# Kernel optimization log

Hardware: AMD Instinct MI355X
Metric: run time of the kernel (lower is better)

Reference implementation:

```python
import jax, jax.numpy as jnp
import numpy as np

D_MODEL = 1024
HEADS = 16
D_K = D_MODEL // HEADS


def setup_inputs() -> dict:
    key = jax.random.key(0)
    ks = jax.random.split(key, 11)
    B, S = 4, 2048
    s = 1.0 / np.sqrt(D_MODEL)
    return {
        "q": jax.random.normal(ks[0], (B, S, D_MODEL), dtype=jnp.float32),
        "k": jax.random.normal(ks[1], (B, S, D_MODEL), dtype=jnp.float32),
        "v": jax.random.normal(ks[2], (B, S, D_MODEL), dtype=jnp.float32),
        "Wq": jax.random.normal(ks[3], (D_MODEL, D_MODEL), dtype=jnp.float32) * s,
        "bq": jnp.zeros((D_MODEL,), dtype=jnp.float32),
        "Wk": jax.random.normal(ks[4], (D_MODEL, D_MODEL), dtype=jnp.float32) * s,
        "bk": jnp.zeros((D_MODEL,), dtype=jnp.float32),
        "Wv": jax.random.normal(ks[5], (D_MODEL, D_MODEL), dtype=jnp.float32) * s,
        "bv": jnp.zeros((D_MODEL,), dtype=jnp.float32),
        "Wo": jax.random.normal(ks[6], (D_MODEL, D_MODEL), dtype=jnp.float32) * s,
        "bo": jnp.zeros((D_MODEL,), dtype=jnp.float32),
    }


def reference(q, k, v, Wq, bq, Wk, bk, Wv, bv, Wo, bo):
    B, S, _ = q.shape
    # projections -> [B, H, S, d_k]
    def proj(x, W, b):
        return (x @ W.T + b).reshape(B, -1, HEADS, D_K).transpose(0, 2, 1, 3)
    qh = proj(q, Wq, bq)
    kh = proj(k, Wk, bk)
    vh = proj(v, Wv, bv)
    scores = jnp.einsum("bhqd,bhkd->bhqk", qh, kh) / jnp.sqrt(jnp.float32(D_K))
    attn = jax.nn.softmax(scores, axis=-1)  # dropout is identity in eval mode
    out = jnp.einsum("bhqk,bhkd->bhqd", attn, vh)
    concat = out.transpose(0, 2, 1, 3).reshape(B, S, D_MODEL)
    return concat @ Wo.T + bo
```

## Files before the change

kernel.cpp:

```cpp
#include <hip/hip_runtime.h>
#include <hip/hip_bf16.h>


typedef __attribute__((ext_vector_type(8))) short bf16x8;
typedef __attribute__((ext_vector_type(4))) float f32x4;
typedef __attribute__((ext_vector_type(4))) float fvec4;
typedef __attribute__((ext_vector_type(4))) unsigned int uvec4;
typedef __attribute__((ext_vector_type(4))) unsigned short usvec4;

#define MFMA16(a, b, c) __builtin_amdgcn_mfma_f32_16x16x32_bf16((a), (b), (c), 0, 0, 0)

static __device__ __forceinline__ unsigned short f2bf(float f) {
  unsigned u = __builtin_bit_cast(unsigned, f);
  unsigned r = u + 0x7FFFu + ((u >> 16) & 1u);
  return (unsigned short)(r >> 16);
}
static __device__ __forceinline__ float bf2f(unsigned short h) {
  unsigned u = ((unsigned)h) << 16;
  return __builtin_bit_cast(float, u);
}
static __device__ __forceinline__ void split2(float x, unsigned short& hi, unsigned short& lo) {
  hi = f2bf(x);
  lo = f2bf(x - bf2f(hi));
}
static __device__ __forceinline__ unsigned int split_pack(float x) {
  unsigned short hi, lo;
  split2(x, hi, lo);
  return ((unsigned)lo << 16) | (unsigned)hi;
}

static __device__ __forceinline__ int swz(int row, int col_us) {
  return (row << 6) + ((((col_us >> 3) ^ row) & 7) << 3) + (col_us & 7);
}

static __device__ __forceinline__ void glds16(const void* g, void* l) {
  __builtin_amdgcn_global_load_lds(
      (const __attribute__((address_space(1))) void*)g,
      (__attribute__((address_space(3))) void*)l, 16, 0, 0);
}

__global__ __launch_bounds__(256) void convert_split(
    const float* __restrict__ in, unsigned short* __restrict__ hp,
    unsigned short* __restrict__ lp, int n) {
  const int i = (blockIdx.x * 256 + threadIdx.x) * 4;
  if (i >= n) return;
  fvec4 x = *reinterpret_cast<const fvec4*>(&in[i]);
  usvec4 h, l;
#pragma unroll
  for (int j = 0; j < 4; ++j) {
    unsigned short hi, lo;
    split2(x[j], hi, lo);
    h[j] = hi; l[j] = lo;
  }
  *reinterpret_cast<usvec4*>(&hp[i]) = h;
  *reinterpret_cast<usvec4*>(&lp[i]) = l;
}

template <int AMODE, int BMODE, int OMODE>
__global__ __launch_bounds__(256) void gemm_k(
    const void* __restrict__ Ap0, const void* __restrict__ Ap1,
    const void* __restrict__ Bp0, const void* __restrict__ Bp1,
    const float* __restrict__ bias, void* __restrict__ Cout,
    int M, int N, int K) {
  __shared__ unsigned short Ahi[128 * 64], Alo[128 * 64];
  __shared__ unsigned short Bhi[128 * 64], Blo[128 * 64];

  const int t = threadIdx.x;
  const int l = t & 63;
  const int w = t >> 6;
  const int g = l >> 4;
  const int r16 = l & 15;
  const int wr = w >> 1, wc = w & 1;

  const int m0 = blockIdx.y * 128;
  const int n0 = blockIdx.x * 128;

  const int srow = t >> 4;
  const int scol = (t & 15) * 4;
  const int glrow = l >> 3;
  const int glcol = ((l & 7) ^ glrow) * 8;

  f32x4 acc[4][4];
#pragma unroll
  for (int m = 0; m < 4; ++m)
#pragma unroll
    for (int n = 0; n < 4; ++n) acc[m][n] = (f32x4){0.f, 0.f, 0.f, 0.f};

  const int ksteps = K / 64;
  for (int kt = 0; kt < ksteps; ++kt) {
    if constexpr (AMODE == 2) {
#pragma unroll
      for (int c = 0; c < 4; ++c) {
        const int row = (c * 4 + w) * 8 + glrow;
        const size_t go = (size_t)(m0 + row) * K + kt * 64 + glcol;
        glds16(&((const unsigned short*)Ap0)[go], &Ahi[(c * 4 + w) * 512]);
        glds16(&((const unsigned short*)Ap1)[go], &Alo[(c * 4 + w) * 512]);
      }
    }
    if constexpr (BMODE == 1) {
#pragma unroll
      for (int c = 0; c < 4; ++c) {
        const int row = (c * 4 + w) * 8 + glrow;
        const size_t go = (size_t)(n0 + row) * K + kt * 64 + glcol;
        glds16(&((const unsigned short*)Bp0)[go], &Bhi[(c * 4 + w) * 512]);
        glds16(&((const unsigned short*)Bp1)[go], &Blo[(c * 4 + w) * 512]);
      }
    }
    if constexpr (AMODE <= 1 || BMODE == 0) {
#pragma unroll
      for (int p = 0; p < 8; ++p) {
        const int row = srow + p * 16;
        const int o = swz(row, scol);
        if constexpr (AMODE == 0) {
          fvec4 av = *reinterpret_cast<const fvec4*>(
              &((const float*)Ap0)[(size_t)(m0 + row) * K + kt * 64 + scol]);
          usvec4 ah, al;
#pragma unroll
          for (int j = 0; j < 4; ++j) {
            unsigned short h, lo;
            split2(av[j], h, lo);
            ah[j] = h; al[j] = lo;
          }
          *reinterpret_cast<usvec4*>(&Ahi[o]) = ah;
          *reinterpret_cast<usvec4*>(&Alo[o]) = al;
        } else if constexpr (AMODE == 1) {
          uvec4 av = *reinterpret_cast<const uvec4*>(
              &((const unsigned int*)Ap0)[(size_t)(m0 + row) * K + kt * 64 + scol]);
          usvec4 ah, al;
#pragma unroll
          for (int j = 0; j < 4; ++j) {
            ah[j] = (unsigned short)(av[j] & 0xFFFFu);
            al[j] = (unsigned short)(av[j] >> 16);
          }
          *reinterpret_cast<usvec4*>(&Ahi[o]) = ah;
          *reinterpret_cast<usvec4*>(&Alo[o]) = al;
        }
        if constexpr (BMODE == 0) {
          fvec4 wv = *reinterpret_cast<const fvec4*>(
              &((const float*)Bp0)[(size_t)(n0 + row) * K + kt * 64 + scol]);
          usvec4 bh, bl;
#pragma unroll
          for (int j = 0; j < 4; ++j) {
            unsigned short h, lo;
            split2(wv[j], h, lo);
            bh[j] = h; bl[j] = lo;
          }
          *reinterpret_cast<usvec4*>(&Bhi[o]) = bh;
          *reinterpret_cast<usvec4*>(&Blo[o]) = bl;
        }
      }
    }
    __syncthreads();

#pragma unroll
    for (int ks = 0; ks < 2; ++ks) {
      bf16x8 ah[4], al[4], bh[4], bl[4];
#pragma unroll
      for (int m = 0; m < 4; ++m) {
        const int o = swz(wr * 64 + m * 16 + r16, ks * 32 + g * 8);
        ah[m] = *reinterpret_cast<const bf16x8*>(&Ahi[o]);
        al[m] = *reinterpret_cast<const bf16x8*>(&Alo[o]);
      }
#pragma unroll
      for (int n = 0; n < 4; ++n) {
        const int o = swz(wc * 64 + n * 16 + r16, ks * 32 + g * 8);
        bh[n] = *reinterpret_cast<const bf16x8*>(&Bhi[o]);
        bl[n] = *reinterpret_cast<const bf16x8*>(&Blo[o]);
      }
#pragma unroll
      for (int m = 0; m < 4; ++m)
#pragma unroll
        for (int n = 0; n < 4; ++n) {
          acc[m][n] = MFMA16(al[m], bh[n], acc[m][n]);
          acc[m][n] = MFMA16(ah[m], bl[n], acc[m][n]);
          acc[m][n] = MFMA16(ah[m], bh[n], acc[m][n]);
        }
    }
    __syncthreads();
  }

  float bv[4];
#pragma unroll
  for (int n = 0; n < 4; ++n) bv[n] = bias[n0 + wc * 64 + n * 16 + r16];

#pragma unroll
  for (int m = 0; m < 4; ++m)
#pragma unroll
    for (int n = 0; n < 4; ++n)
#pragma unroll
      for (int r = 0; r < 4; ++r) {
        const int row = m0 + wr * 64 + m * 16 + g * 4 + r;
        const int col = n0 + wc * 64 + n * 16 + r16;
        const float c = acc[m][n][r] + bv[n];
        if constexpr (OMODE == 0) {
          ((float*)Cout)[(size_t)row * N + col] = c;
        } else if constexpr (OMODE == 1) {
          ((unsigned int*)Cout)[(size_t)row * N + col] = split_pack(c);
        } else {
          ((unsigned int*)Cout)[(size_t)row * N + col] = split_pack(c * 0.125f);
        }
      }
}

template <int OPL>
__global__ __launch_bounds__(256) void attn_fwd(
    const unsigned int* Qpk, const unsigned int* __restrict__ Kpk,
    const unsigned int* __restrict__ Vpk, unsigned int* CtxPk,
    unsigned short* CtxH, unsigned short* CtxL, int S) {
  constexpr int DM = 1024, DK = 64;
  __shared__ unsigned short Khi[64 * 64], Klo[64 * 64];
  __shared__ unsigned short Vth[64 * 64], Vtl[64 * 64];
  __shared__ unsigned short Ph[4 * 16 * 64], Pl[4 * 16 * 64];

  const int t = threadIdx.x;
  const int l = t & 63;
  const int w = t >> 6;
  const int g = l >> 4;
  const int r16 = l & 15;
  const int pw = w << 10;

  const int b = blockIdx.z, h = blockIdx.y;
  const int q0 = blockIdx.x * 128;

  bf16x8 qhi[2][2], qlo[2][2];
#pragma unroll
  for (int qq = 0; qq < 2; ++qq)
#pragma unroll
    for (int ks = 0; ks < 2; ++ks) {
      const unsigned int* qrow =
          &Qpk[(size_t)(b * S + q0 + qq * 64 + w * 16 + r16) * DM + h * DK + ks * 32 + g * 8];
      uvec4 u0 = *reinterpret_cast<const uvec4*>(qrow);
      uvec4 u1 = *reinterpret_cast<const uvec4*>(qrow + 4);
#pragma unroll
      for (int j = 0; j < 4; ++j) {
        qhi[qq][ks][j] = (short)(u0[j] & 0xFFFFu);
        qlo[qq][ks][j] = (short)(u0[j] >> 16);
        qhi[qq][ks][4 + j] = (short)(u1[j] & 0xFFFFu);
        qlo[qq][ks][4 + j] = (short)(u1[j] >> 16);
      }
    }

  f32x4 o[2][4];
#pragma unroll
  for (int qq = 0; qq < 2; ++qq)
#pragma unroll
    for (int nf = 0; nf < 4; ++nf) o[qq][nf] = (f32x4){0.f, 0.f, 0.f, 0.f};
  float mrow[2][4], lrow[2][4];
#pragma unroll
  for (int qq = 0; qq < 2; ++qq)
#pragma unroll
    for (int r = 0; r < 4; ++r) { mrow[qq][r] = -1e30f; lrow[qq][r] = 0.f; }

  const int srow = t >> 4;
  const int scol = (t & 15) * 4;
  const int s4 = l >> 4;
  const bool sb1 = (s4 >> 1) & 1;
  const bool sb0 = s4 & 1;

  uvec4 kreg[4], vreg[4];

  auto LOADTILE = [&](int kt) {
#pragma unroll
    for (int p = 0; p < 4; ++p) {
      const size_t gb = (size_t)(b * S + kt * 64 + srow + p * 16) * DM + h * DK + scol;
      kreg[p] = *reinterpret_cast<const uvec4*>(&Kpk[gb]);
      vreg[p] = *reinterpret_cast<const uvec4*>(&Vpk[gb]);
    }
  };
  auto WRITETILE = [&]() {
#pragma unroll
    for (int p = 0; p < 4; ++p) {
      const int row = srow + p * 16;
      usvec4 kh, kl;
#pragma unroll
      for (int j = 0; j < 4; ++j) {
        kh[j] = (unsigned short)(kreg[p][j] & 0xFFFFu);
        kl[j] = (unsigned short)(kreg[p][j] >> 16);
      }
      const int ko = swz(row, scol);
      *reinterpret_cast<usvec4*>(&Khi[ko]) = kh;
      *reinterpret_cast<usvec4*>(&Klo[ko]) = kl;

      unsigned int pv0 = vreg[p][0], pv1 = vreg[p][1];
      unsigned int pv2 = vreg[p][2], pv3 = vreg[p][3];
      {
        unsigned int t0 = sb1 ? pv0 : pv2;
        unsigned int t1 = sb1 ? pv1 : pv3;
        unsigned int r0 = __shfl_xor((int)t0, 32);
        unsigned int r1 = __shfl_xor((int)t1, 32);
        if (sb1) { pv0 = r0; pv1 = r1; } else { pv2 = r0; pv3 = r1; }
      }
      {
        unsigned int t0 = sb0 ? pv0 : pv1;
        unsigned int t1 = sb0 ? pv2 : pv3;
        unsigned int r0 = __shfl_xor((int)t0, 16);
        unsigned int r1 = __shfl_xor((int)t1, 16);
        if (sb0) { pv0 = r0; pv2 = r1; } else { pv1 = r0; pv3 = r1; }
      }
      const int d = 4 * r16 + s4;
      const int kb = p * 16 + w * 4;
      usvec4 vh, vl;
      vh[0] = (unsigned short)(pv0 & 0xFFFFu); vl[0] = (unsigned short)(pv0 >> 16);
      vh[1] = (unsigned short)(pv1 & 0xFFFFu); vl[1] = (unsigned short)(pv1 >> 16);
      vh[2] = (unsigned short)(pv2 & 0xFFFFu); vl[2] = (unsigned short)(pv2 >> 16);
      vh[3] = (unsigned short)(pv3 & 0xFFFFu); vl[3] = (unsigned short)(pv3 >> 16);
      const int vo = swz(d, kb);
      *reinterpret_cast<usvec4*>(&Vth[vo]) = vh;
      *reinterpret_cast<usvec4*>(&Vtl[vo]) = vl;
    }
  };

  LOADTILE(0);
  WRITETILE();
  __syncthreads();

  const int nt = S / 64;
  for (int kt = 0; kt < nt; ++kt) {
    if (kt + 1 < nt) LOADTILE(kt + 1);

#pragma unroll
    for (int qq = 0; qq < 2; ++qq) {
      f32x4 s[4];
#pragma unroll
      for (int nf = 0; nf < 4; ++nf) s[nf] = (f32x4){0.f, 0.f, 0.f, 0.f};
      __builtin_amdgcn_s_setprio(1);
#pragma unroll
      for (int ks = 0; ks < 2; ++ks) {
#pragma unroll
        for (int nf = 0; nf < 4; ++nf) {
          const int o2 = swz(nf * 16 + r16, ks * 32 + g * 8);
          bf16x8 kh = *reinterpret_cast<const bf16x8*>(&Khi[o2]);
          bf16x8 kl = *reinterpret_cast<const bf16x8*>(&Klo[o2]);
          s[nf] = MFMA16(qlo[qq][ks], kh, s[nf]);
          s[nf] = MFMA16(qhi[qq][ks], kl, s[nf]);
          s[nf] = MFMA16(qhi[qq][ks], kh, s[nf]);
        }
      }
      __builtin_amdgcn_s_setprio(0);

#pragma unroll
      for (int r = 0; r < 4; ++r) {
        float sm = fmaxf(fmaxf(s[0][r], s[1][r]), fmaxf(s[2][r], s[3][r]));
        sm = fmaxf(sm, __shfl_xor(sm, 1));
        sm = fmaxf(sm, __shfl_xor(sm, 2));
        sm = fmaxf(sm, __shfl_xor(sm, 4));
        sm = fmaxf(sm, __shfl_xor(sm, 8));
        const float mnew = fmaxf(mrow[qq][r], sm);
        const float f = __expf(mrow[qq][r] - mnew);
        mrow[qq][r] = mnew;
        float rs = 0.f;
#pragma unroll
        for (int nf = 0; nf < 4; ++nf) {
          const float p = __expf(s[nf][r] - mnew);
          s[nf][r] = p;
          rs += p;
        }
        rs += __shfl_xor(rs, 1);
        rs += __shfl_xor(rs, 2);
        rs += __shfl_xor(rs, 4);
        rs += __shfl_xor(rs, 8);
        lrow[qq][r] = lrow[qq][r] * f + rs;
#pragma unroll
        for (int nf = 0; nf < 4; ++nf) o[qq][nf][r] *= f;
      }

#pragma unroll
      for (int nf = 0; nf < 4; ++nf)
#pragma unroll
        for (int r = 0; r < 4; ++r) {
          unsigned short hi, lo;
          split2(s[nf][r], hi, lo);
          const int po = pw + swz(g * 4 + r, nf * 16 + r16);
          Ph[po] = hi;
          Pl[po] = lo;
        }

      __builtin_amdgcn_s_setprio(1);
#pragma unroll
      for (int ks = 0; ks < 2; ++ks) {
        const int po = pw + swz(r16, ks * 32 + g * 8);
        bf16x8 ph = *reinterpret_cast<const bf16x8*>(&Ph[po]);
        bf16x8 pl = *reinterpret_cast<const bf16x8*>(&Pl[po]);
#pragma unroll
        for (int nf = 0; nf < 4; ++nf) {
          const int vo = swz(nf * 16 + r16, ks * 32 + g * 8);
          bf16x8 vh = *reinterpret_cast<const bf16x8*>(&Vth[vo]);
          bf16x8 vl = *reinterpret_cast<const bf16x8*>(&Vtl[vo]);
          o[qq][nf] = MFMA16(pl, vh, o[qq][nf]);
          o[qq][nf] = MFMA16(ph, vl, o[qq][nf]);
          o[qq][nf] = MFMA16(ph, vh, o[qq][nf]);
        }
      }
      __builtin_amdgcn_s_setprio(0);
    }
    __syncthreads();
    if (kt + 1 < nt) WRITETILE();
    __syncthreads();
  }

#pragma unroll
  for (int qq = 0; qq < 2; ++qq)
#pragma unroll
    for (int r = 0; r < 4; ++r) {
      const float inv = 1.0f / lrow[qq][r];
      const int row = q0 + qq * 64 + w * 16 + g * 4 + r;
#pragma unroll
      for (int nf = 0; nf < 4; ++nf) {
        const size_t idx = ((size_t)b * S + row) * DM + h * DK + nf * 16 + r16;
        const float val = o[qq][nf][r] * inv;
        if constexpr (OPL == 0) {
          CtxPk[idx] = split_pack(val);
        } else {
          unsigned short hi, lo;
          split2(val, hi, lo);
          CtxH[idx] = hi;
          CtxL[idx] = lo;
        }
      }
    }
}

extern "C" void kernel_launch(void* const* d_in, const int* in_sizes, int n_in,
                              void* d_out, int out_size, void* d_ws, size_t ws_size,
                              hipStream_t stream) {
  const float* q  = (const float*)d_in[0];
  const float* k  = (const float*)d_in[1];
  const float* v  = (const float*)d_in[2];
  const float* Wq = (const float*)d_in[3];
  const float* bq = (const float*)d_in[4];
  const float* Wk = (const float*)d_in[5];
  const float* bk = (const float*)d_in[6];
  const float* Wv = (const float*)d_in[7];
  const float* bv = (const float*)d_in[8];
  const float* Wo = (const float*)d_in[9];
  const float* bo = (const float*)d_in[10];

  const int DM = 1024;
  const int S = 2048;
  const int BS = in_sizes[0] / DM;
  const int B = BS / S;
  const size_t MB = 1024 * 1024;

  const int NW = DM * DM;
  const int NI = BS * DM;
  const int cgW = NW / (256 * 4);
  const int cgI = NI / (256 * 4);
  dim3 ggrid(DM / 128, BS / 128);
  dim3 agrid(S / 128, 16, B);

  char* wsb = (char*)d_ws;

  if (ws_size >= 144 * MB) {
    unsigned short* Th = (unsigned short*)(wsb);
    unsigned short* Tl = (unsigned short*)(wsb + 16 * MB);
    unsigned int* Qpk = (unsigned int*)(wsb + 32 * MB);
    unsigned int* Kpk = (unsigned int*)(wsb + 64 * MB);
    unsigned int* Vpk = (unsigned int*)(wsb + 96 * MB);
    unsigned short* Wp = (unsigned short*)(wsb + 128 * MB);
    unsigned short *Wqh = Wp + 0 * MB, *Wql = Wp + 1 * MB;
    unsigned short *Wkh = Wp + 2 * MB, *Wkl = Wp + 3 * MB;
    unsigned short *Wvh = Wp + 4 * MB, *Wvl = Wp + 5 * MB;
    unsigned short *Woh = Wp + 6 * MB, *Wol = Wp + 7 * MB;

    convert_split<<<cgW, 256, 0, stream>>>(Wq, Wqh, Wql, NW);
    convert_split<<<cgW, 256, 0, stream>>>(Wk, Wkh, Wkl, NW);
    convert_split<<<cgW, 256, 0, stream>>>(Wv, Wvh, Wvl, NW);
    convert_split<<<cgW, 256, 0, stream>>>(Wo, Woh, Wol, NW);

    convert_split<<<cgI, 256, 0, stream>>>(q, Th, Tl, NI);
    gemm_k<2, 1, 2><<<ggrid, 256, 0, stream>>>(Th, Tl, Wqh, Wql, bq, Qpk, BS, DM, DM);
    convert_split<<<cgI, 256, 0, stream>>>(k, Th, Tl, NI);
    gemm_k<2, 1, 1><<<ggrid, 256, 0, stream>>>(Th, Tl, Wkh, Wkl, bk, Kpk, BS, DM, DM);
    convert_split<<<cgI, 256, 0, stream>>>(v, Th, Tl, NI);
    gemm_k<2, 1, 1><<<ggrid, 256, 0, stream>>>(Th, Tl, Wvh, Wvl, bv, Vpk, BS, DM, DM);

    attn_fwd<1><<<agrid, 256, 0, stream>>>(Qpk, Kpk, Vpk, nullptr, Th, Tl, S);

    gemm_k<2, 1, 0><<<ggrid, 256, 0, stream>>>(Th, Tl, Woh, Wol, bo, d_out, BS, DM, DM);
  } else if (ws_size >= 112 * MB) {
    unsigned int* Qpk = (unsigned int*)(wsb);
    unsigned int* Kpk = (unsigned int*)(wsb + 32 * MB);
    unsigned int* Vpk = (unsigned int*)(wsb + 64 * MB);
    unsigned short* Wp = (unsigned short*)(wsb + 96 * MB);
    unsigned short *Wqh = Wp + 0 * MB, *Wql = Wp + 1 * MB;
    unsigned short *Wkh = Wp + 2 * MB, *Wkl = Wp + 3 * MB;
    unsigned short *Wvh = Wp + 4 * MB, *Wvl = Wp + 5 * MB;
    unsigned short *Woh = Wp + 6 * MB, *Wol = Wp + 7 * MB;

    convert_split<<<cgW, 256, 0, stream>>>(Wq, Wqh, Wql, NW);
    convert_split<<<cgW, 256, 0, stream>>>(Wk, Wkh, Wkl, NW);
    convert_split<<<cgW, 256, 0, stream>>>(Wv, Wvh, Wvl, NW);
    convert_split<<<cgW, 256, 0, stream>>>(Wo, Woh, Wol, NW);

    gemm_k<0, 1, 2><<<ggrid, 256, 0, stream>>>(q, nullptr, Wqh, Wql, bq, Qpk, BS, DM, DM);
    gemm_k<0, 1, 1><<<ggrid, 256, 0, stream>>>(k, nullptr, Wkh, Wkl, bk, Kpk, BS, DM, DM);
    gemm_k<0, 1, 1><<<ggrid, 256, 0, stream>>>(v, nullptr, Wvh, Wvl, bv, Vpk, BS, DM, DM);

    attn_fwd<0><<<agrid, 256, 0, stream>>>(Qpk, Kpk, Vpk, Qpk, nullptr, nullptr, S);

    gemm_k<1, 1, 0><<<ggrid, 256, 0, stream>>>(Qpk, nullptr, Woh, Wol, bo, d_out, BS, DM, DM);
  } else {
    unsigned int* Qpk = (unsigned int*)(wsb);
    unsigned int* Kpk = (unsigned int*)(wsb + 32 * MB);
    unsigned int* Vpk = (unsigned int*)(wsb + 64 * MB);

    gemm_k<0, 0, 2><<<ggrid, 256, 0, stream>>>(q, nullptr, Wq, nullptr, bq, Qpk, BS, DM, DM);
    gemm_k<0, 0, 1><<<ggrid, 256, 0, stream>>>(k, nullptr, Wk, nullptr, bk, Kpk, BS, DM, DM);
    gemm_k<0, 0, 1><<<ggrid, 256, 0, stream>>>(v, nullptr, Wv, nullptr, bv, Vpk, BS, DM, DM);

    attn_fwd<0><<<agrid, 256, 0, stream>>>(Qpk, Kpk, Vpk, Qpk, nullptr, nullptr, S);

    gemm_k<1, 0, 0><<<ggrid, 256, 0, stream>>>(Qpk, nullptr, Wo, nullptr, bo, d_out, BS, DM, DM);
  }
}
```

Measured before the change: 766.4 us.

## Transpose score MFMA so each lane owns a row and skip unchanged max rescales

Swaps the MFMA operand order for the QK^T product so the score tile comes out transposed. Each lane then holds all 16 scores of one query row locally, and the per-row max and sum need only two cross-lane shuffles instead of four shuffles repeated per row. It also adds a wave-uniform check that skips the online-softmax rescale of the output accumulator when no row max increased. The P write to LDS is re-indexed for the new layout, and the rescale and normalisation factors are broadcast back to the output layout with shuffles. This adds some index and shuffle overhead and a divergent branch.

```diff
diff --git a/kernel.cpp b/kernel.cpp
--- a/kernel.cpp
+++ b/kernel.cpp
@@ -245,11 +245,8 @@
   for (int qq = 0; qq < 2; ++qq)
 #pragma unroll
     for (int nf = 0; nf < 4; ++nf) o[qq][nf] = (f32x4){0.f, 0.f, 0.f, 0.f};
-  float mrow[2][4], lrow[2][4];
-#pragma unroll
-  for (int qq = 0; qq < 2; ++qq)
-#pragma unroll
-    for (int r = 0; r < 4; ++r) { mrow[qq][r] = -1e30f; lrow[qq][r] = 0.f; }
+  float m_sm[2] = {-1e30f, -1e30f};
+  float l_sm[2] = {0.f, 0.f};
 
   const int srow = t >> 4;
   const int scol = (t & 15) * 4;
@@ -322,55 +319,65 @@
     for (int qq = 0; qq < 2; ++qq) {
       f32x4 s[4];
 #pragma unroll
-      for (int nf = 0; nf < 4; ++nf) s[nf] = (f32x4){0.f, 0.f, 0.f, 0.f};
+      for (int i = 0; i < 4; ++i) s[i] = (f32x4){0.f, 0.f, 0.f, 0.f};
       __builtin_amdgcn_s_setprio(1);
 #pragma unroll
       for (int ks = 0; ks < 2; ++ks) {
 #pragma unroll
-        for (int nf = 0; nf < 4; ++nf) {
-          const int o2 = swz(nf * 16 + r16, ks * 32 + g * 8);
+        for (int i = 0; i < 4; ++i) {
+          const int o2 = swz(i * 16 + r16, ks * 32 + g * 8);
           bf16x8 kh = *reinterpret_cast<const bf16x8*>(&Khi[o2]);
           bf16x8 kl = *reinterpret_cast<const bf16x8*>(&Klo[o2]);
-          s[nf] = MFMA16(qlo[qq][ks], kh, s[nf]);
-          s[nf] = MFMA16(qhi[qq][ks], kl, s[nf]);
-          s[nf] = MFMA16(qhi[qq][ks], kh, s[nf]);
+          s[i] = MFMA16(kh, qlo[qq][ks], s[i]);
+          s[i] = MFMA16(kl, qhi[qq][ks], s[i]);
+          s[i] = MFMA16(kh, qhi[qq][ks], s[i]);
         }
       }
       __builtin_amdgcn_s_setprio(0);
 
-#pragma unroll
-      for (int r = 0; r < 4; ++r) {
-        float sm = fmaxf(fmaxf(s[0][r], s[1][r]), fmaxf(s[2][r], s[3][r]));
-        sm = fmaxf(sm, __shfl_xor(sm, 1));
-        sm = fmaxf(sm, __shfl_xor(sm, 2));
-        sm = fmaxf(sm, __shfl_xor(sm, 4));
-        sm = fmaxf(sm, __shfl_xor(sm, 8));
-        const float mnew = fmaxf(mrow[qq][r], sm);
-        const float f = __expf(mrow[qq][r] - mnew);
-        mrow[qq][r] = mnew;
-        float rs = 0.f;
-#pragma unroll
-        for (int nf = 0; nf < 4; ++nf) {
-          const float p = __expf(s[nf][r] - mnew);
-          s[nf][r] = p;
+      f32x4 x0, x1;
+#pragma unroll
+      for (int r = 0; r < 4; ++r) x0[r] = fmaxf(s[0][r], s[1][r]);
+#pragma unroll
+      for (int r = 0; r < 4; ++r) x1[r] = fmaxf(s[2][r], s[3][r]);
+      float pm = fmaxf(fmaxf(fmaxf(x0[0], x0[1]), fmaxf(x0[2], x0[3])),
+                       fmaxf(fmaxf(x1[0], x1[1]), fmaxf(x1[2], x1[3])));
+      pm = fmaxf(pm, __shfl_xor(pm, 16));
+      pm = fmaxf(pm, __shfl_xor(pm, 32));
+
+      if (!__all(pm <= m_sm[qq])) {
+        const float mnew = fmaxf(m_sm[qq], pm);
+        const float f = __expf(m_sm[qq] - mnew);
+        m_sm[qq] = mnew;
+        l_sm[qq] *= f;
+#pragma unroll
+        for (int r = 0; r < 4; ++r) {
+          const float fr = __shfl(f, (l & 48) | (4 * g + r));
+#pragma unroll
+          for (int nf = 0; nf < 4; ++nf) o[qq][nf][r] *= fr;
+        }
+      }
+
+      float rs = 0.f;
+#pragma unroll
+      for (int i = 0; i < 4; ++i)
+#pragma unroll
+        for (int r = 0; r < 4; ++r) {
+          const float p = __expf(s[i][r] - m_sm[qq]);
+          s[i][r] = p;
           rs += p;
         }
-        rs += __shfl_xor(rs, 1);
-        rs += __shfl_xor(rs, 2);
-        rs += __shfl_xor(rs, 4);
-        rs += __shfl_xor(rs, 8);
-        lrow[qq][r] = lrow[qq][r] * f + rs;
-#pragma unroll
-        for (int nf = 0; nf < 4; ++nf) o[qq][nf][r] *= f;
-      }
-
-#pragma unroll
-      for (int nf = 0; nf < 4; ++nf)
+      rs += __shfl_xor(rs, 16);
+      rs += __shfl_xor(rs, 32);
+      l_sm[qq] += rs;
+
+#pragma unroll
+      for (int i = 0; i < 4; ++i)
 #pragma unroll
         for (int r = 0; r < 4; ++r) {
           unsigned short hi, lo;
-          split2(s[nf][r], hi, lo);
-          const int po = pw + swz(g * 4 + r, nf * 16 + r16);
+          split2(s[i][r], hi, lo);
+          const int po = pw + swz(r16, i * 16 + 4 * g + r);
           Ph[po] = hi;
           Pl[po] = lo;
         }
@@ -399,15 +406,16 @@
   }
 
 #pragma unroll
-  for (int qq = 0; qq < 2; ++qq)
+  for (int qq = 0; qq < 2; ++qq) {
+    const float inv = 1.0f / l_sm[qq];
 #pragma unroll
     for (int r = 0; r < 4; ++r) {
-      const float inv = 1.0f / lrow[qq][r];
+      const float ir = __shfl(inv, (l & 48) | (4 * g + r));
       const int row = q0 + qq * 64 + w * 16 + g * 4 + r;
 #pragma unroll
       for (int nf = 0; nf < 4; ++nf) {
         const size_t idx = ((size_t)b * S + row) * DM + h * DK + nf * 16 + r16;
-        const float val = o[qq][nf][r] * inv;
+        const float val = o[qq][nf][r] * ir;
         if constexpr (OPL == 0) {
           CtxPk[idx] = split_pack(val);
         } else {
@@ -418,6 +426,7 @@
         }
       }
     }
+  }
 }
 
 extern "C" void kernel_launch(void* const* d_in, const int* in_sizes, int n_in,
```

Result: faster. 699.6 us (-8.7%).
